# Performance work log

Measured on AMD Instinct MI355X. Metric: run time of the kernel, lower is better.

Reference implementation:

```python
import jax, jax.numpy as jnp
import numpy as np

# ---- static dims (from init_kwargs) ----
B, V, G, NH, C = 2, 3, 2, 8, 128
CPG, CH, HPG = C // G, C // NH, NH // G          # 64, 16, 4
Hq = Wq = 32
D = 4                                            # bev_depth_dim
Hk, Wk = Hq // 2, Wq * D                         # 16, 128 (per rearrange)
NS = Hk * Wk                                     # n_sample = 2048
Hi = Wi = 64
SCALE = CH ** -0.5
OFR = 5.0                                        # offset_range_factor
EPS = 1e-5


def grid_sample_bilinear(img, grid):
    """torch.F.grid_sample(mode='bilinear', align_corners=True, padding='zeros').
    img: (N, Cc, H, W); grid: (N, Hg, Wg, 2) with (x, y) in [-1, 1]."""
    N, Cc, H, W = img.shape
    x = (grid[..., 0] + 1.0) * 0.5 * (W - 1)
    y = (grid[..., 1] + 1.0) * 0.5 * (H - 1)
    x0 = jnp.floor(x); y0 = jnp.floor(y)
    wx1 = x - x0; wy1 = y - y0
    wx0 = 1.0 - wx1; wy0 = 1.0 - wy1

    def gather(ix, iy):
        valid = ((ix >= 0) & (ix <= W - 1) & (iy >= 0) & (iy <= H - 1)).astype(img.dtype)
        ixc = jnp.clip(ix, 0, W - 1).astype(jnp.int32)
        iyc = jnp.clip(iy, 0, H - 1).astype(jnp.int32)
        vals = jax.vmap(lambda im, yy, xx: im[:, yy, xx])(img, iyc, ixc)  # (N,Cc,Hg,Wg)
        return vals * valid[:, None]

    return (gather(x0, y0) * (wx0 * wy0)[:, None]
            + gather(x0 + 1.0, y0) * (wx1 * wy0)[:, None]
            + gather(x0, y0 + 1.0) * (wx0 * wy1)[:, None]
            + gather(x0 + 1.0, y0 + 1.0) * (wx1 * wy1)[:, None])


def offset_net(qg, w1, b1, gln, bln, w2):
    """Depthwise 1x1 conv (groups=CPG, fan-out D) -> channel LayerNorm -> GELU -> 1x1 conv.
    qg: (B*G, CPG, Hq, Wq) -> (B*G, D, Hq, Wq)."""
    h = qg[:, :, None] * w1.reshape(CPG, D)[None, :, :, None, None] \
        + b1.reshape(CPG, D)[None, :, :, None, None]
    h = h.reshape(B * G, CPG * D, Hq, Wq)
    mu = h.mean(axis=1, keepdims=True)
    var = h.var(axis=1, keepdims=True)           # biased, like torch LayerNorm
    h = (h - mu) * jax.lax.rsqrt(var + EPS) * gln[None, :, None, None] + bln[None, :, None, None]
    h = jax.nn.gelu(h, approximate=False)
    return jnp.einsum('oc,bchw->bohw', w2, h)


def _q_grid():
    gy, gx = jnp.meshgrid(jnp.linspace(-1.0, 1.0, Hq), jnp.linspace(-1.0, 1.0, Wq), indexing='ij')
    return jnp.stack([gy, gx], -1)               # (Hq, Wq, 2) in (y, x)


def setup_inputs() -> dict:
    key = jax.random.key(0)
    ks = jax.random.split(key, 15)
    s = 0.05
    return {
        'x': jax.random.normal(ks[0], (B, V, C, Hi, Wi), jnp.float32),
        'query': jax.random.normal(ks[1], (B, C, Hq, Wq), jnp.float32),
        'reference_points': jax.random.uniform(ks[2], (B, V, Hk, Wk, 2), jnp.float32) * 2.0 - 1.0,
        'off_w1': jax.random.normal(ks[3], (V, CPG * D), jnp.float32) * s,
        'off_b1': jax.random.normal(ks[4], (V, CPG * D), jnp.float32) * s,
        'off_ln_g': jnp.ones((V, CPG * D), jnp.float32),
        'off_ln_b': jnp.zeros((V, CPG * D), jnp.float32),
        'off_w2': jax.random.normal(ks[5], (V, D, CPG * D), jnp.float32) * s,
        'k_w': jax.random.normal(ks[6], (C, C), jnp.float32) * s,
        'k_b': jnp.zeros((C,), jnp.float32),
        'v_w': jax.random.normal(ks[7], (C, C), jnp.float32) * s,
        'v_b': jnp.zeros((C,), jnp.float32),
        'out_w': jax.random.normal(ks[8], (C, C * V), jnp.float32) * s,
        'out_b': jnp.zeros((C,), jnp.float32),
        'rpe_table': jax.random.normal(ks[9], (NH, Hq * 2 - 1, Wq * D * 2 - 1), jnp.float32) * 0.01,
    }


def reference(x, query, reference_points, off_w1, off_b1, off_ln_g, off_ln_b, off_w2,
              k_w, k_b, v_w, v_b, out_w, out_b, rpe_table):
    ref = reference_points[..., ::-1]                     # (x,y) -> (y,x)
    ref = jnp.repeat(ref, G, axis=0)                      # (B*G, V, Hk, Wk, 2)
    q_g = query.reshape(B, G, CPG, Hq, Wq).reshape(B * G, CPG, Hq, Wq)
    q = query.reshape(B * NH, CH, Hq * Wq)
    qg = _q_grid().reshape(1, Hq * Wq, 2)
    off_rng = jnp.array([1.0 / (Hk - 1.0), 1.0 / (Wk - 1.0)], jnp.float32).reshape(1, 2, 1, 1)
    rpe = jnp.broadcast_to(rpe_table[None], (B,) + rpe_table.shape)
    rpe = rpe.reshape(B * G, HPG, rpe_table.shape[1], rpe_table.shape[2])

    outs = []
    for vi in range(V):
        off = offset_net(q_g, off_w1[vi], off_b1[vi], off_ln_g[vi], off_ln_b[vi], off_w2[vi])
        # rearrange '(b g) d (h n) w -> (b g) n h (w d)'
        off = off.reshape(B * G, D, Hk, 2, Wq).transpose(0, 3, 2, 4, 1).reshape(B * G, 2, Hk, Wk)
        off = jnp.tanh(off) * off_rng * OFR
        off = off.transpose(0, 2, 3, 1)                   # (B*G, Hk, Wk, 2) in (y, x)
        rwo = off + ref[:, vi]                            # scale_offset_range=True -> no clamp
        xs = grid_sample_bilinear(x[:, vi].reshape(B * G, CPG, Hi, Wi), rwo[..., ::-1])
        xs = xs.reshape(B, C, NS)
        k = (jnp.einsum('oc,bcn->bon', k_w, xs) + k_b[None, :, None]).reshape(B * NH, CH, NS)
        vv = (jnp.einsum('oc,bcn->bon', v_w, xs) + v_b[None, :, None]).reshape(B * NH, CH, NS)
        attn = jnp.einsum('bcm,bcn->bmn', q, k) * SCALE   # (B*NH, m, NS)
        disp = (qg[:, :, None] - rwo.reshape(B * G, NS, 2)[:, None]) * 0.5  # (B*G, m, NS, 2)
        bias = grid_sample_bilinear(rpe, disp[..., ::-1]).reshape(B * NH, Hq * Wq, NS)
        attn = jax.nn.softmax(attn + bias, axis=-1)
        outs.append(jnp.einsum('bmn,bcn->bcm', attn, vv).reshape(B, C, Hq, Wq))

    out = jnp.concatenate(outs, axis=1)                   # (B, V*C, Hq, Wq)
    return jnp.einsum('oc,bchw->bohw', out_w, out) + out_b[None, :, None, None]
```

## Files before the change

kernel.cpp:

```cpp
#include <hip/hip_runtime.h>
#include <hip/hip_bf16.h>
#include <math.h>


typedef __attribute__((ext_vector_type(8))) short short8;
typedef __attribute__((ext_vector_type(4))) float f32x4;

__device__ __forceinline__ unsigned short f2b(float f){
  unsigned u = __float_as_uint(f);
  return (unsigned short)((u + 0x7FFFu + ((u>>16)&1u)) >> 16);
}
__device__ __forceinline__ unsigned pack2(float lo, float hi){
  return (unsigned)f2b(lo) | ((unsigned)f2b(hi) << 16);
}

__global__ void k_probe(float* __restrict__ out, float code){
  if(blockIdx.x==0 && threadIdx.x==0) out[0] = code;
}

__global__ __launch_bounds__(256) void k_prep_off(
    const float* __restrict__ query, const float* __restrict__ refp,
    const float* __restrict__ w1, const float* __restrict__ b1,
    const float* __restrict__ lng, const float* __restrict__ lnb,
    const float* __restrict__ w2, float* __restrict__ rwo, float* __restrict__ rws,
    const float* __restrict__ x, float* __restrict__ xt,
    const float* __restrict__ k_w, const float* __restrict__ v_w, const float* __restrict__ out_w,
    unsigned short* __restrict__ kw16, unsigned short* __restrict__ vw16, float* __restrict__ ow_t){
  __shared__ float t[64][65];
  int bx = blockIdx.x;
  if(bx < 3072){
    int wid  = bx*4 + (threadIdx.x>>6);
    int lane = threadIdx.x & 63;
    int vi  = wid >> 12;
    int rem = wid & 4095;
    int bg  = rem >> 10;
    int pix = rem & 1023;
    int y = pix >> 5, xq = pix & 31;
    int b = bg >> 1, g = bg & 1;
    float qv = query[(size_t)(b*128 + g*64 + lane)*1024 + pix];
    float h[4]; float s1 = 0.f, s2 = 0.f;
    #pragma unroll
    for(int d=0; d<4; ++d){
      h[d] = qv*w1[vi*256 + lane*4 + d] + b1[vi*256 + lane*4 + d];
      s1 += h[d]; s2 += h[d]*h[d];
    }
    #pragma unroll
    for(int off=1; off<64; off<<=1){ s1 += __shfl_xor(s1, off); s2 += __shfl_xor(s2, off); }
    float mu   = s1 * (1.f/256.f);
    float var  = s2 * (1.f/256.f) - mu*mu;
    float rstd = rsqrtf(fmaxf(var, 0.f) + 1e-5f);
    float po[4] = {0.f,0.f,0.f,0.f};
    #pragma unroll
    for(int d=0; d<4; ++d){
      float hv = (h[d]-mu)*rstd*lng[vi*256+lane*4+d] + lnb[vi*256+lane*4+d];
      hv = 0.5f*hv*(1.f + erff(hv*0.70710678118654752f));
      #pragma unroll
      for(int o=0; o<4; ++o) po[o] += w2[(vi*4+o)*256 + lane*4 + d] * hv;
    }
    #pragma unroll
    for(int off=1; off<64; off<<=1){
      #pragma unroll
      for(int o=0; o<4; ++o) po[o] += __shfl_xor(po[o], off);
    }
    if(lane == 0){
      int tt = y & 1, hk = y >> 1;
      float rng = tt ? (5.f/127.f) : (5.f/15.f);
      float csc = tt ? 63.5f : 15.5f;
      #pragma unroll
      for(int d=0; d<4; ++d){
        int wk = xq*4 + d;
        float rv = refp[(size_t)(((b*3+vi)*16 + hk)*128 + wk)*2 + (1-tt)];
        float coord = tanhf(po[d])*rng + rv;
        size_t o2 = ((size_t)(vi*4+bg)*2048 + hk*128 + wk)*2 + tt;
        rwo[o2] = coord;
        rws[o2] = coord * csc;
      }
    }
  } else if(bx < 3840){
    int pb = bx - 3072;
    int iy = pb & 63;
    int o2 = pb >> 6;
    const float* src = x + ((size_t)o2*64)*4096 + (size_t)iy*64;
    int ix = threadIdx.x & 63, cq = threadIdx.x >> 6;
    #pragma unroll
    for(int c0 = 0; c0 < 64; c0 += 4)
      t[c0+cq][ix] = src[(size_t)(c0+cq)*4096 + ix];
    __syncthreads();
    float* dst = xt + (((size_t)o2*64 + iy)*64)*64;
    int c = threadIdx.x & 63, xq = threadIdx.x >> 6;
    #pragma unroll
    for(int x0 = 0; x0 < 64; x0 += 4)
      dst[(size_t)(x0+xq)*64 + c] = t[c][x0+xq];
  } else {
    int wb = bx - 3840;
    if(wb < 128){
      int i = (wb & 63)*256 + threadIdx.x;
      if(wb < 64) kw16[i] = f2b(k_w[i]);
      else        vw16[i] = f2b(v_w[i]);
    } else {
      int i = (wb-128)*256 + threadIdx.x;
      if(i < 49152){
        int r = i / 384, c = i - r*384;
        ow_t[c*128 + r] = out_w[i];
      }
    }
  }
}

__global__ __launch_bounds__(256) void k_sampro(
    const float* __restrict__ rwo, const float* __restrict__ xt,
    const unsigned short* __restrict__ kw16, const float* __restrict__ k_b,
    const unsigned short* __restrict__ vw16, const float* __restrict__ v_b,
    unsigned short* __restrict__ k_b16, unsigned short* __restrict__ v_t16){
  __shared__ alignas(16) unsigned short tile[16*136];
  int bx = blockIdx.x;
  int nt = bx & 127;
  int r2 = bx >> 7;
  int b = r2 & 1, vi = r2 >> 1;
  int n0 = nt*16;
  int tid = threadIdx.x, wid = tid>>6, lane = tid&63;
  #pragma unroll
  for(int s = 0; s < 8; ++s){
    int u = wid*8 + s;
    int nl = u >> 1, g = u & 1;
    int n = n0 + nl;
    float yn = rwo[((size_t)(vi*4 + b*2 + g)*2048 + n)*2 + 0];
    float xn = rwo[((size_t)(vi*4 + b*2 + g)*2048 + n)*2 + 1];
    float px = (xn + 1.f)*31.5f;
    float py = (yn + 1.f)*31.5f;
    float x0 = floorf(px), y0 = floorf(py);
    float fx = px - x0, fy = py - y0;
    int ix0 = (int)x0, iy0 = (int)y0;
    const float* base = xt + (size_t)((b*3+vi)*2+g)*4096*64;
    float wts[4] = {(1.f-fx)*(1.f-fy), fx*(1.f-fy), (1.f-fx)*fy, fx*fy};
    int ixs[4] = {ix0, ix0+1, ix0, ix0+1};
    int iys[4] = {iy0, iy0, iy0+1, iy0+1};
    float acc = 0.f;
    #pragma unroll
    for(int tp=0; tp<4; ++tp){
      int ix = ixs[tp], iy = iys[tp];
      if(ix>=0 && ix<64 && iy>=0 && iy<64)
        acc += wts[tp] * base[(size_t)((iy<<6)+ix)*64 + lane];
    }
    tile[nl*136 + g*64 + lane] = f2b(acc);
  }
  __syncthreads();
  int c = lane & 15, qd = lane >> 4;
  short8 af[4];
  #pragma unroll
  for(int kc=0; kc<4; ++kc)
    af[kc] = *(const short8*)(&tile[c*136 + kc*32 + qd*8]);
  size_t vbbase = (size_t)(vi*16 + b*8)*2048*16;
  #pragma unroll
  for(int half=0; half<2; ++half){
    int nh = wid*2 + half;
    size_t hbase = vbbase + (size_t)nh*2048*16;
    {
      f32x4 C = {0.f,0.f,0.f,0.f};
      #pragma unroll
      for(int kc=0; kc<4; ++kc){
        short8 bf = *(const short8*)(kw16 + (size_t)(nh*16 + c)*128 + kc*32 + qd*8);
        C = __builtin_amdgcn_mfma_f32_16x16x32_bf16(af[kc], bf, C, 0, 0, 0);
      }
      float bias = k_b[nh*16 + c];
      #pragma unroll
      for(int r=0; r<4; ++r)
        k_b16[hbase + (size_t)(n0 + qd*4 + r)*16 + c] = f2b(C[r] + bias);
    }
    {
      f32x4 C = {0.f,0.f,0.f,0.f};
      #pragma unroll
      for(int kc=0; kc<4; ++kc){
        short8 bf = *(const short8*)(vw16 + (size_t)(nh*16 + c)*128 + kc*32 + qd*8);
        C = __builtin_amdgcn_mfma_f32_16x16x32_bf16(af[kc], bf, C, 0, 0, 0);
      }
      float bias = v_b[nh*16 + c];
      uint2 pk;
      pk.x = pack2(C[0]+bias, C[1]+bias);
      pk.y = pack2(C[2]+bias, C[3]+bias);
      *(uint2*)(v_t16 + hbase + (size_t)c*2048 + n0 + qd*4) = pk;
    }
  }
}

__global__ __launch_bounds__(256,3) void k_attn(
    const float* __restrict__ rws, const unsigned short* __restrict__ k_b16,
    const unsigned short* __restrict__ v_t16, const float* __restrict__ query,
    const float* __restrict__ rpe, float* __restrict__ attn_pc){
  __shared__ unsigned P32[47*258];
  __shared__ alignas(16) short p_sm[4][16*40];
  int bx = blockIdx.x;
  int vi = bx >> 8;
  int bh = (bx >> 4) & 15;
  int mblk = bx & 15;
  int b = bh >> 3, nh = bh & 7, g = nh >> 2, bg = b*2 + g;
  int tid = threadIdx.x, wid = tid >> 6;
  int lane = tid & 63, c = lane & 15, qd = lane >> 4;
  int m0 = mblk*64 + wid*16;
  float gy0 = -1.f + (2.f/31.f)*(float)(mblk*2);
  float pyL = 15.5f*(gy0 - 4.f/3.f) + 31.f - 0.01f;
  float pyH = 15.5f*(gy0 + 2.f/31.f + 4.f/3.f) + 31.f + 0.01f;
  int a  = max(-1, (int)floorf(pyL));
  int bb = min(63, (int)floorf(pyH));
  int iy_lo = max(a - 1, bb - 46);
  {
    const float* rt = rpe + (size_t)nh*16065;
    for(int e = tid; e < 12126; e += 256){
      int rr = e / 258;
      int cc = e - rr*258;
      int iy = iy_lo + rr;
      int ix = cc - 1;
      bool xv = (ix >= 0) && (ix <= 254);
      float lo = (xv && iy   >= 0 && iy   <= 62) ? rt[iy*255 + ix]     : 0.f;
      float hi = (xv && iy+1 >= 0 && iy+1 <= 62) ? rt[(iy+1)*255 + ix] : 0.f;
      P32[e] = pack2(lo*1.44269504f, hi*1.44269504f);
    }
  }
  short8 qa;
  #pragma unroll
  for(int j=0; j<8; ++j){
    int ch = qd*8 + j;
    qa[j] = (qd < 2) ? (short)f2b(query[(size_t)(b*128 + nh*16 + ch)*1024 + m0 + c]) : (short)0;
  }
  float Ax2[4], Ay2[4];
  #pragma unroll
  for(int r=0; r<4; ++r){
    int mr = m0 + qd*4 + r;
    float gxr = -1.f + (2.f/31.f)*(mr & 31);
    float gyr = -1.f + (2.f/31.f)*(mr >> 5);
    Ax2[r] = 63.5f*gxr + 128.f;
    Ay2[r] = 15.5f*gyr + 31.f - (float)iy_lo;
  }
  float loC = -1.f - (float)iy_lo, hiC = 63.f - (float)iy_lo;
  const float SC2 = 0.36067376022224085f;
  float si[4] = {0.f, 0.f, 0.f, 0.f};
  f32x4 O = {0.f, 0.f, 0.f, 0.f};
  size_t kvb  = (size_t)(vi*16 + bh)*2048*16;
  size_t rwsb = (size_t)(vi*4 + bg)*2048;
  __syncthreads();
  for(int nc = 0; nc < 16; ++nc){
    int n0 = nc*128;
    f32x4 Sf[8];
    #pragma unroll
    for(int t=0; t<8; ++t){
      short8 bk = {0,0,0,0,0,0,0,0};
      if(qd < 2) bk = *(const short8*)(k_b16 + kvb + (size_t)(n0 + t*16 + c)*16 + qd*8);
      f32x4 z = {0.f,0.f,0.f,0.f};
      Sf[t] = __builtin_amdgcn_mfma_f32_16x16x32_bf16(qa, bk, z, 0, 0, 0);
    }
    unsigned short pb[8][4];
    #pragma unroll
    for(int t=0; t<8; ++t){
      float2 rs = *(const float2*)(rws + (rwsb + n0 + t*16 + c)*2);
      float ysc = rs.x, xsc = rs.y;
      #pragma unroll
      for(int r=0; r<4; ++r){
        float px = Ax2[r] - xsc;
        float py = Ay2[r] - ysc;
        px = fminf(fmaxf(px, 0.f), 256.f);
        py = fminf(fmaxf(py, loC), hiC);
        float cf = floorf(px), rf = floorf(py);
        float fx = px - cf, fy = py - rf;
        int idx = (int)rf * 258 + (int)cf;
        unsigned w0 = P32[idx], w1 = P32[idx+1];
        float lo0 = __uint_as_float(w0 << 16), hi0 = __uint_as_float(w0 & 0xFFFF0000u);
        float lo1 = __uint_as_float(w1 << 16), hi1 = __uint_as_float(w1 & 0xFFFF0000u);
        float t0 = lo0 + fy*(hi0 - lo0);
        float t1 = lo1 + fy*(hi1 - lo1);
        float p = exp2f(Sf[t][r]*SC2 + t0 + fx*(t1 - t0));
        si[r] += p;
        pb[t][r] = f2b(p);
      }
    }
    short* pw = &p_sm[wid][0];
    #pragma unroll
    for(int kc=0; kc<4; ++kc){
      #pragma unroll
      for(int tt=0; tt<2; ++tt){
        int t = kc*2 + tt;
        #pragma unroll
        for(int r=0; r<4; ++r)
          pw[(qd*4 + r)*40 + tt*16 + c] = (short)pb[t][r];
      }
      short8 va = *(const short8*)(v_t16 + kvb + (size_t)c*2048 + n0 + kc*32 + qd*8);
      short8 pbf = *(const short8*)(&pw[c*40 + qd*8]);
      O = __builtin_amdgcn_mfma_f32_16x16x32_bf16(va, pbf, O, 0, 0, 0);
    }
  }
  #pragma unroll
  for(int r=0; r<4; ++r){
    float sv = si[r];
    sv += __shfl_xor(sv, 1); sv += __shfl_xor(sv, 2);
    sv += __shfl_xor(sv, 4); sv += __shfl_xor(sv, 8);
    si[r] = sv;
  }
  int msrc = (c >> 2)*16 + c;
  int rsel = c & 3;
  float s0 = __shfl(si[0], msrc), s1 = __shfl(si[1], msrc),
        s2 = __shfl(si[2], msrc), s3 = __shfl(si[3], msrc);
  float sv = (rsel==0) ? s0 : ((rsel==1) ? s1 : ((rsel==2) ? s2 : s3));
  float inv = 1.f/sv;
  float4 o4;
  o4.x = O[0]*inv; o4.y = O[1]*inv; o4.z = O[2]*inv; o4.w = O[3]*inv;
  *(float4*)(attn_pc + (size_t)(b*1024 + m0 + c)*384 + vi*128 + nh*16 + qd*4) = o4;
}

__global__ __launch_bounds__(256) void k_outproj(
    const float* __restrict__ attn_pc, const float* __restrict__ ow_t, const float* __restrict__ out_b,
    float* __restrict__ out){
  __shared__ float A[8*384];
  int bx = blockIdx.x;
  int b  = bx >> 7;
  int m0 = (bx & 127)*8;
  const float4* src = (const float4*)(attn_pc + ((size_t)b*1024 + m0)*384);
  float4* dst = (float4*)A;
  for(int i = threadIdx.x; i < 768; i += 256) dst[i] = src[i];
  __syncthreads();
  int oc = threadIdx.x & 127;
  int mh = threadIdx.x >> 7;
  float acc[4] = {0.f,0.f,0.f,0.f};
  for(int vc = 0; vc < 384; ++vc){
    float wv = ow_t[vc*128 + oc];
    #pragma unroll
    for(int j=0; j<4; ++j) acc[j] += wv * A[(mh*4+j)*384 + vc];
  }
  float ob = out_b[oc];
  #pragma unroll
  for(int j=0; j<4; ++j)
    out[((size_t)b*128 + oc)*1024 + m0 + mh*4 + j] = acc[j] + ob;
}

extern "C" void kernel_launch(void* const* d_in, const int* in_sizes, int n_in,
                              void* d_out, int out_size, void* d_ws, size_t ws_size,
                              hipStream_t stream){
  const float* x     = (const float*)d_in[0];
  const float* query = (const float*)d_in[1];
  const float* refp  = (const float*)d_in[2];
  const float* w1    = (const float*)d_in[3];
  const float* b1    = (const float*)d_in[4];
  const float* lng   = (const float*)d_in[5];
  const float* lnb   = (const float*)d_in[6];
  const float* w2    = (const float*)d_in[7];
  const float* k_w   = (const float*)d_in[8];
  const float* k_b   = (const float*)d_in[9];
  const float* v_w   = (const float*)d_in[10];
  const float* v_b   = (const float*)d_in[11];
  const float* out_w = (const float*)d_in[12];
  const float* out_b = (const float*)d_in[13];
  const float* rpe   = (const float*)d_in[14];

  const size_t O_XT   = 0;
  const size_t O_RWO  = 12582912;
  const size_t O_RWS  = 12779520;
  const size_t O_KB16 = 12976128;
  const size_t O_VT16 = 16121856;
  const size_t O_APC  = 19267584;
  const size_t O_KW16 = 22413312;
  const size_t O_VW16 = 22446080;
  const size_t O_OWT  = 22478848;
  const size_t NEED   = 22675456;
  if(ws_size < NEED){
    k_probe<<<1, 64, 0, stream>>>((float*)d_out, 100.f + (float)(ws_size >> 20));
    return;
  }
  char* ws = (char*)d_ws;
  float* xt      = (float*)(ws + O_XT);
  float* rwo     = (float*)(ws + O_RWO);
  float* rws     = (float*)(ws + O_RWS);
  unsigned short* k_b16 = (unsigned short*)(ws + O_KB16);
  unsigned short* v_t16 = (unsigned short*)(ws + O_VT16);
  float* attn_pc = (float*)(ws + O_APC);
  unsigned short* kw16 = (unsigned short*)(ws + O_KW16);
  unsigned short* vw16 = (unsigned short*)(ws + O_VW16);
  float* ow_t    = (float*)(ws + O_OWT);

  k_prep_off<<<4160, 256, 0, stream>>>(query, refp, w1, b1, lng, lnb, w2, rwo, rws,
                                       x, xt, k_w, v_w, out_w, kw16, vw16, ow_t);
  k_sampro  <<<768,  256, 0, stream>>>(rwo, xt, kw16, k_b, vw16, v_b, k_b16, v_t16);
  k_attn    <<<768,  256, 0, stream>>>(rws, k_b16, v_t16, query, rpe, attn_pc);
  k_outproj <<<256,  256, 0, stream>>>(attn_pc, ow_t, out_b, (float*)d_out);
}
```

Before: 271.3 us.

## Precompute packed RPE table globally, restructure attn inner loop, split outproj finer

After: 305.5 us. 1.13x slower.

```diff
diff --git a/kernel.cpp b/kernel.cpp
--- a/kernel.cpp
+++ b/kernel.cpp
@@ -25,7 +25,8 @@
     const float* __restrict__ w2, float* __restrict__ rwo, float* __restrict__ rws,
     const float* __restrict__ x, float* __restrict__ xt,
     const float* __restrict__ k_w, const float* __restrict__ v_w, const float* __restrict__ out_w,
-    unsigned short* __restrict__ kw16, unsigned short* __restrict__ vw16, float* __restrict__ ow_t){
+    unsigned short* __restrict__ kw16, unsigned short* __restrict__ vw16, float* __restrict__ ow_t,
+    const float* __restrict__ rpe, unsigned* __restrict__ gP){
   __shared__ float t[64][65];
   int bx = blockIdx.x;
   if(bx < 3072){
@@ -91,7 +92,7 @@
     #pragma unroll
     for(int x0 = 0; x0 < 64; x0 += 4)
       dst[(size_t)(x0+xq)*64 + c] = t[c][x0+xq];
-  } else {
+  } else if(bx < 4160){
     int wb = bx - 3840;
     if(wb < 128){
       int i = (wb & 63)*256 + threadIdx.x;
@@ -103,6 +104,20 @@
         int r = i / 384, c = i - r*384;
         ow_t[c*128 + r] = out_w[i];
       }
+    }
+  } else {
+    int e = (bx - 4160)*256 + threadIdx.x;
+    if(e < 136224){
+      int nh = e / 17028;
+      int r  = e - nh*17028;
+      int iy = r / 258 - 2;
+      int cc = r - (iy+2)*258;
+      int ix = cc - 1;
+      const float* rt = rpe + (size_t)nh*16065;
+      bool xv = (ix >= 0) && (ix <= 254);
+      float lo = (xv && iy   >= 0 && iy   <= 62) ? rt[iy*255 + ix]     : 0.f;
+      float hi = (xv && iy+1 >= 0 && iy+1 <= 62) ? rt[(iy+1)*255 + ix] : 0.f;
+      gP[e] = pack2(lo*1.44269504f, hi*1.44269504f);
     }
   }
 }
@@ -186,9 +201,9 @@
 __global__ __launch_bounds__(256,3) void k_attn(
     const float* __restrict__ rws, const unsigned short* __restrict__ k_b16,
     const unsigned short* __restrict__ v_t16, const float* __restrict__ query,
-    const float* __restrict__ rpe, float* __restrict__ attn_pc){
-  __shared__ unsigned P32[47*258];
-  __shared__ alignas(16) short p_sm[4][16*40];
+    const unsigned* __restrict__ gP, float* __restrict__ attn_pc){
+  __shared__ alignas(8) unsigned P32[47*258];
+  __shared__ alignas(16) short p_sm[4][16*42];
   int bx = blockIdx.x;
   int vi = bx >> 8;
   int bh = (bx >> 4) & 15;
@@ -202,19 +217,11 @@
   float pyH = 15.5f*(gy0 + 2.f/31.f + 4.f/3.f) + 31.f + 0.01f;
   int a  = max(-1, (int)floorf(pyL));
   int bb = min(63, (int)floorf(pyH));
-  int iy_lo = max(a - 1, bb - 46);
+  int iy_lo = max(bb - 46, min(a - 1, 17));
   {
-    const float* rt = rpe + (size_t)nh*16065;
-    for(int e = tid; e < 12126; e += 256){
-      int rr = e / 258;
-      int cc = e - rr*258;
-      int iy = iy_lo + rr;
-      int ix = cc - 1;
-      bool xv = (ix >= 0) && (ix <= 254);
-      float lo = (xv && iy   >= 0 && iy   <= 62) ? rt[iy*255 + ix]     : 0.f;
-      float hi = (xv && iy+1 >= 0 && iy+1 <= 62) ? rt[(iy+1)*255 + ix] : 0.f;
-      P32[e] = pack2(lo*1.44269504f, hi*1.44269504f);
-    }
+    const uint2* src2 = (const uint2*)(gP + (size_t)nh*17028 + (size_t)(iy_lo+2)*258);
+    uint2* dst2 = (uint2*)P32;
+    for(int i = tid; i < 6063; i += 256) dst2[i] = src2[i];
   }
   short8 qa;
   #pragma unroll
@@ -237,53 +244,48 @@
   f32x4 O = {0.f, 0.f, 0.f, 0.f};
   size_t kvb  = (size_t)(vi*16 + bh)*2048*16;
   size_t rwsb = (size_t)(vi*4 + bg)*2048;
+  short* pw = &p_sm[wid][0];
   __syncthreads();
   for(int nc = 0; nc < 16; ++nc){
     int n0 = nc*128;
-    f32x4 Sf[8];
-    #pragma unroll
-    for(int t=0; t<8; ++t){
-      short8 bk = {0,0,0,0,0,0,0,0};
-      if(qd < 2) bk = *(const short8*)(k_b16 + kvb + (size_t)(n0 + t*16 + c)*16 + qd*8);
-      f32x4 z = {0.f,0.f,0.f,0.f};
-      Sf[t] = __builtin_amdgcn_mfma_f32_16x16x32_bf16(qa, bk, z, 0, 0, 0);
-    }
-    unsigned short pb[8][4];
-    #pragma unroll
-    for(int t=0; t<8; ++t){
-      float2 rs = *(const float2*)(rws + (rwsb + n0 + t*16 + c)*2);
-      float ysc = rs.x, xsc = rs.y;
-      #pragma unroll
-      for(int r=0; r<4; ++r){
-        float px = Ax2[r] - xsc;
-        float py = Ay2[r] - ysc;
-        px = fminf(fmaxf(px, 0.f), 256.f);
-        py = fminf(fmaxf(py, loC), hiC);
-        float cf = floorf(px), rf = floorf(py);
-        float fx = px - cf, fy = py - rf;
-        int idx = (int)rf * 258 + (int)cf;
-        unsigned w0 = P32[idx], w1 = P32[idx+1];
-        float lo0 = __uint_as_float(w0 << 16), hi0 = __uint_as_float(w0 & 0xFFFF0000u);
-        float lo1 = __uint_as_float(w1 << 16), hi1 = __uint_as_float(w1 & 0xFFFF0000u);
-        float t0 = lo0 + fy*(hi0 - lo0);
-        float t1 = lo1 + fy*(hi1 - lo1);
-        float p = exp2f(Sf[t][r]*SC2 + t0 + fx*(t1 - t0));
-        si[r] += p;
-        pb[t][r] = f2b(p);
-      }
-    }
-    short* pw = &p_sm[wid][0];
-    #pragma unroll
-    for(int kc=0; kc<4; ++kc){
+    const unsigned short* kbase = k_b16 + kvb + (size_t)n0*16;
+    const unsigned short* vbase = v_t16 + kvb + (size_t)c*2048 + n0;
+    const float* rbase = rws + (rwsb + n0)*2;
+    #pragma unroll
+    for(int hf = 0; hf < 4; ++hf){
+      f32x4 S[2];
       #pragma unroll
       for(int tt=0; tt<2; ++tt){
-        int t = kc*2 + tt;
+        short8 bk = {0,0,0,0,0,0,0,0};
+        if(qd < 2) bk = *(const short8*)(kbase + (size_t)((hf*2+tt)*16 + c)*16 + qd*8);
+        f32x4 z = {0.f,0.f,0.f,0.f};
+        S[tt] = __builtin_amdgcn_mfma_f32_16x16x32_bf16(qa, bk, z, 0, 0, 0);
+      }
+      #pragma unroll
+      for(int tt=0; tt<2; ++tt){
+        float2 rs = *(const float2*)(rbase + ((hf*2+tt)*16 + c)*2);
+        float ysc = rs.x, xsc = rs.y;
         #pragma unroll
-        for(int r=0; r<4; ++r)
-          pw[(qd*4 + r)*40 + tt*16 + c] = (short)pb[t][r];
-      }
-      short8 va = *(const short8*)(v_t16 + kvb + (size_t)c*2048 + n0 + kc*32 + qd*8);
-      short8 pbf = *(const short8*)(&pw[c*40 + qd*8]);
+        for(int r=0; r<4; ++r){
+          float px = Ax2[r] - xsc;
+          float py = Ay2[r] - ysc;
+          px = fminf(fmaxf(px, 0.f), 256.f);
+          py = fminf(fmaxf(py, loC), hiC);
+          float cf = floorf(px), rf = floorf(py);
+          float fx = px - cf, fy = py - rf;
+          int idx = (int)rf * 258 + (int)cf;
+          unsigned w0 = P32[idx], w1 = P32[idx+1];
+          float lo0 = __uint_as_float(w0 << 16), hi0 = __uint_as_float(w0 & 0xFFFF0000u);
+          float lo1 = __uint_as_float(w1 << 16), hi1 = __uint_as_float(w1 & 0xFFFF0000u);
+          float t0 = lo0 + fy*(hi0 - lo0);
+          float t1 = lo1 + fy*(hi1 - lo1);
+          float p = exp2f(S[tt][r]*SC2 + t0 + fx*(t1 - t0));
+          si[r] += p;
+          pw[(qd*4 + r)*42 + tt*16 + c] = (short)f2b(p);
+        }
+      }
+      short8 va  = *(const short8*)(vbase + hf*32 + qd*8);
+      short8 pbf = *(const short8*)(&pw[c*42 + qd*8]);
       O = __builtin_amdgcn_mfma_f32_16x16x32_bf16(va, pbf, O, 0, 0, 0);
     }
   }
@@ -308,26 +310,26 @@
 __global__ __launch_bounds__(256) void k_outproj(
     const float* __restrict__ attn_pc, const float* __restrict__ ow_t, const float* __restrict__ out_b,
     float* __restrict__ out){
-  __shared__ float A[8*384];
+  __shared__ float A[4*384];
   int bx = blockIdx.x;
-  int b  = bx >> 7;
-  int m0 = (bx & 127)*8;
+  int b  = bx >> 8;
+  int m0 = (bx & 255)*4;
   const float4* src = (const float4*)(attn_pc + ((size_t)b*1024 + m0)*384);
   float4* dst = (float4*)A;
-  for(int i = threadIdx.x; i < 768; i += 256) dst[i] = src[i];
+  for(int i = threadIdx.x; i < 384; i += 256) dst[i] = src[i];
   __syncthreads();
   int oc = threadIdx.x & 127;
   int mh = threadIdx.x >> 7;
-  float acc[4] = {0.f,0.f,0.f,0.f};
+  float acc[2] = {0.f, 0.f};
   for(int vc = 0; vc < 384; ++vc){
     float wv = ow_t[vc*128 + oc];
     #pragma unroll
-    for(int j=0; j<4; ++j) acc[j] += wv * A[(mh*4+j)*384 + vc];
+    for(int j=0; j<2; ++j) acc[j] += wv * A[(mh*2+j)*384 + vc];
   }
   float ob = out_b[oc];
   #pragma unroll
-  for(int j=0; j<4; ++j)
-    out[((size_t)b*128 + oc)*1024 + m0 + mh*4 + j] = acc[j] + ob;
+  for(int j=0; j<2; ++j)
+    out[((size_t)b*128 + oc)*1024 + m0 + mh*2 + j] = acc[j] + ob;
 }
 
 extern "C" void kernel_launch(void* const* d_in, const int* in_sizes, int n_in,
@@ -358,7 +360,8 @@
   const size_t O_KW16 = 22413312;
   const size_t O_VW16 = 22446080;
   const size_t O_OWT  = 22478848;
-  const size_t NEED   = 22675456;
+  const size_t O_GPT  = 22675456;
+  const size_t NEED   = 23220352;
   if(ws_size < NEED){
     k_probe<<<1, 64, 0, stream>>>((float*)d_out, 100.f + (float)(ws_size >> 20));
     return;
@@ -373,10 +376,11 @@
   unsigned short* kw16 = (unsigned short*)(ws + O_KW16);
   unsigned short* vw16 = (unsigned short*)(ws + O_VW16);
   float* ow_t    = (float*)(ws + O_OWT);
-
-  k_prep_off<<<4160, 256, 0, stream>>>(query, refp, w1, b1, lng, lnb, w2, rwo, rws,
-                                       x, xt, k_w, v_w, out_w, kw16, vw16, ow_t);
+  unsigned* gP   = (unsigned*)(ws + O_GPT);
+
+  k_prep_off<<<4693, 256, 0, stream>>>(query, refp, w1, b1, lng, lnb, w2, rwo, rws,
+                                       x, xt, k_w, v_w, out_w, kw16, vw16, ow_t, rpe, gP);
   k_sampro  <<<768,  256, 0, stream>>>(rwo, xt, kw16, k_b, vw16, v_b, k_b16, v_t16);
-  k_attn    <<<768,  256, 0, stream>>>(rws, k_b16, v_t16, query, rpe, attn_pc);
-  k_outproj <<<256,  256, 0, stream>>>(attn_pc, ow_t, out_b, (float*)d_out);
-}
+  k_attn    <<<768,  256, 0, stream>>>(rws, k_b16, v_t16, query, gP, attn_pc);
+  k_outproj <<<512,  256, 0, stream>>>(attn_pc, ow_t, out_b, (float*)d_out);
+}
```
